# Kernel optimization log

Hardware: AMD Instinct MI355X
Metric: run time of the kernel (lower is better)

Reference implementation:

```python
import jax, jax.numpy as jnp
import numpy as np

B, HC, WC, KC = 4, 32, 32, 1024   # coarse feature map (ResNet101 layer3)
HF, WF, KF = 128, 128, 256        # fine feature map (ResNet101 layer1)
DC = 4                            # downscale_coef; HF // DC == HC


def setup_inputs() -> dict:
    key = jax.random.key(0)
    k1, k2, k3, k4 = jax.random.split(key, 4)
    return {
        "F_g1_coarse": jax.random.normal(k1, (B, HC, WC, KC), jnp.float32),
        "F_gk_coarse": jax.random.normal(k2, (B, HC, WC, KC), jnp.float32),
        "F_g1_fine": jax.random.normal(k3, (B, HF, WF, KF), jnp.float32),
        "F_gk_fine": jax.random.normal(k4, (B, HF, WF, KF), jnp.float32),
    }


def _coarse_match(f1, fk):
    # For every coarse position in Gk find nearest (L2) coarse position in G1.
    b, h, w, k = f1.shape
    a = f1.reshape(b, h * w, k)   # G1 positions
    q = fk.reshape(b, h * w, k)   # Gk positions
    # ||q||^2 + ||a||^2 - 2 q.a  -> [B, HW_gk, HW_g1]
    d = ((q * q).sum(-1)[:, :, None]
         + (a * a).sum(-1)[:, None, :]
         - 2.0 * jnp.einsum('bnk,bmk->bnm', q, a))
    idx = jnp.argmin(d, axis=-1)                       # [B, HW]
    cm = jnp.stack([idx // w, idx % w], axis=-1)       # (row, col) in G1
    return cm.reshape(b, h, w, 2).astype(jnp.int32)


def _fine_match(f1, fk, cm, dc):
    # Refine each dc x dc fine tile of Gk by searching the fine pixels of G1
    # covered by the coarse matches of the 3x3 coarse-neighborhood.
    b, h, w, k = fk.shape
    hc, wc = h // dc, w // dc
    off = jnp.arange(-1, 2)
    nI = jnp.clip(jnp.arange(hc)[:, None] + off[None, :], 0, hc - 1)  # [Hc,3]
    nJ = jnp.clip(jnp.arange(wc)[:, None] + off[None, :], 0, wc - 1)  # [Wc,3]
    # neighbor coarse matches: [B, Hc, Wc, 3, 3, 2]
    nb = cm[:, nI[:, None, :, None], nJ[None, :, None, :]]
    nb = nb.reshape(b, hc, wc, 9, 2)
    # expand each coarse match to its dc*dc fine pixels in G1
    sr = jnp.repeat(jnp.arange(dc), dc)   # [dc^2] row shifts
    sc = jnp.tile(jnp.arange(dc), dc)     # [dc^2] col shifts
    ncand = 9 * dc * dc                   # 144 candidates per tile
    cand_r = (nb[..., 0][..., None] * dc + sr).reshape(b, hc, wc, ncand)
    cand_c = (nb[..., 1][..., None] * dc + sc).reshape(b, hc, wc, ncand)
    # gather candidate fine features from G1: [B, Hc, Wc, N, K]
    bi = jnp.arange(b)[:, None, None, None]
    cand_f = f1[bi, cand_r, cand_c]
    # fine tile features of Gk: [B, Hc, Wc, dc^2, K]
    fkb = fk.reshape(b, hc, dc, wc, dc, k).transpose(0, 1, 3, 2, 4, 5)
    fkb = fkb.reshape(b, hc, wc, dc * dc, k)
    dist = ((fkb * fkb).sum(-1)[..., :, None]
            + (cand_f * cand_f).sum(-1)[..., None, :]
            - 2.0 * jnp.einsum('bhwpk,bhwnk->bhwpn', fkb, cand_f))
    best = jnp.argmin(dist, axis=-1)      # [B, Hc, Wc, dc^2]
    hi = jnp.arange(hc)[None, :, None, None]
    wi = jnp.arange(wc)[None, None, :, None]
    best_r = cand_r[bi, hi, wi, best]     # [B, Hc, Wc, dc^2]
    best_c = cand_c[bi, hi, wi, best]
    def to_grid(x):
        return x.reshape(b, hc, wc, dc, dc).transpose(0, 1, 3, 2, 4).reshape(b, h, w)
    return jnp.stack([to_grid(best_r), to_grid(best_c)], axis=-1).astype(jnp.int32)


def reference(F_g1_coarse, F_gk_coarse, F_g1_fine, F_gk_fine):
    closest_coarse = _coarse_match(F_g1_coarse, F_gk_coarse)   # [B,Hc,Wc,2]
    closest_fine = _fine_match(F_g1_fine, F_gk_fine, closest_coarse, DC)  # [B,H,W,2]
    return closest_coarse, closest_fine
```

## Files before the change

kernel.cpp:

```cpp
#include <hip/hip_runtime.h>
#include <cstdint>
#include <cstddef>

#define BB 4
#define HCC 32
#define WCC 32
#define KCC 1024
#define NCC (HCC*WCC)
#define HFF 128
#define WFF 128
#define KFF 256
#define DCC 4
#define NCHUNK 8

typedef _Float16 half8 __attribute__((ext_vector_type(8)));
typedef _Float16 half4_t __attribute__((ext_vector_type(4)));
typedef float f32x4 __attribute__((ext_vector_type(4)));
#define MFMA16(a,b,c) __builtin_amdgcn_mfma_f32_16x16x32_f16((a),(b),(c),0,0,0)
#define INV2K 0.00048828125f

__device__ inline void cvt8(const float4 u0, const float4 u1, half8& h, half8& l2) {
  float uu[8];
  *(float4*)uu = u0; *(float4*)(uu + 4) = u1;
  #pragma unroll
  for (int e = 0; e < 8; ++e) {
    _Float16 hh = (_Float16)uu[e];
    float r = (uu[e] - (float)hh) * 2048.0f;
    h[e] = hh; l2[e] = (_Float16)r;
  }
}

template<int K>
__global__ __launch_bounds__(256) void preconv_kernel(
    const float* __restrict__ src0, const float* __restrict__ src1,
    _Float16* __restrict__ hi0, _Float16* __restrict__ lo0,
    _Float16* __restrict__ hi1, _Float16* __restrict__ lo1,
    float* __restrict__ nr0, float* __restrict__ nr1, int rows) {
  const float* __restrict__ src = blockIdx.y ? src1 : src0;
  _Float16* __restrict__ hi = blockIdx.y ? hi1 : hi0;
  _Float16* __restrict__ lo = blockIdx.y ? lo1 : lo0;
  float* __restrict__ nrm = blockIdx.y ? nr1 : nr0;
  const int wave = threadIdx.x >> 6, lane = threadIdx.x & 63;
  const int row = blockIdx.x * 4 + wave;
  if (row >= rows) return;
  const float* p = src + (size_t)row * K;
  const size_t ob = (size_t)row * K + lane * 4;
  float s = 0.f;
  #pragma unroll
  for (int c = 0; c < K / 256; ++c) {
    float4 v = *(const float4*)(p + c * 256 + lane * 4);
    s += v.x*v.x + v.y*v.y + v.z*v.z + v.w*v.w;
    float vv[4] = {v.x, v.y, v.z, v.w};
    half4_t h, l2;
    #pragma unroll
    for (int e = 0; e < 4; ++e) {
      _Float16 hh = (_Float16)vv[e];
      l2[e] = (_Float16)((vv[e] - (float)hh) * 2048.0f);
      h[e] = hh;
    }
    *(half4_t*)(hi + ob + c * 256) = h;
    *(half4_t*)(lo + ob + c * 256) = l2;
  }
  #pragma unroll
  for (int m = 1; m <= 32; m <<= 1) s += __shfl_xor(s, m, 64);
  if (lane == 0) nrm[row] = s;
}

__global__ __launch_bounds__(256) void preconv_fine_kernel(
    const float* __restrict__ src, _Float16* __restrict__ hl,
    float* __restrict__ nrm, int rows) {
  const int wave = threadIdx.x >> 6, lane = threadIdx.x & 63;
  const int row = blockIdx.x * 4 + wave;
  if (row >= rows) return;
  float4 v = *(const float4*)(src + (size_t)row * KFF + lane * 4);
  float s = v.x*v.x + v.y*v.y + v.z*v.z + v.w*v.w;
  float vv[4] = {v.x, v.y, v.z, v.w};
  half4_t h, l2;
  #pragma unroll
  for (int e = 0; e < 4; ++e) {
    _Float16 hh = (_Float16)vv[e];
    l2[e] = (_Float16)((vv[e] - (float)hh) * 2048.0f);
    h[e] = hh;
  }
  const size_t dst = (size_t)row * 512 + (lane >> 3) * 64 + ((lane >> 1) & 3) * 16 + (lane & 1) * 4;
  *(half4_t*)(hl + dst)     = h;
  *(half4_t*)(hl + dst + 8) = l2;
  #pragma unroll
  for (int m = 1; m <= 32; m <<= 1) s += __shfl_xor(s, m, 64);
  if (lane == 0) nrm[row] = s;
}

__global__ __launch_bounds__(256) void coarse_kernel3(
    const _Float16* __restrict__ gAhi, const _Float16* __restrict__ gAlo,
    const _Float16* __restrict__ gBhi, const _Float16* __restrict__ gBlo,
    const float* __restrict__ na, const float* __restrict__ nq,
    float* __restrict__ pval, int* __restrict__ pidx) {
  __shared__ _Float16 Ahi[128][64], Alo[128][64];
  __shared__ _Float16 Bhi[64][64],  Blo[64][64];
  __shared__ float a2s[128], q2s[64];
  __shared__ float redv[2][64];
  __shared__ int   redi[2][64];

  const int t = threadIdx.x;
  const int chunk = blockIdx.x;
  const int n0 = blockIdx.y * 64;
  const int b  = blockIdx.z;
  const int m0 = chunk * 128;

  const int ar = t >> 1, ahf = t & 1;
  const int brw = t >> 2, bq = t & 3;
  const int l  = t & 63;
  const int wv = t >> 6;
  const int wm = wv >> 1, wn = wv & 1;

  if (t < 128) a2s[t] = na[b*NCC + m0 + t];
  else if (t < 192) q2s[t - 128] = nq[b*NCC + n0 + (t - 128)];

  const _Float16* __restrict__ gah = gAhi + (size_t)(b*NCC + m0 + ar) * KCC + ahf * 32;
  const _Float16* __restrict__ gal = gAlo + (size_t)(b*NCC + m0 + ar) * KCC + ahf * 32;
  const _Float16* __restrict__ gbh = gBhi + (size_t)(b*NCC + n0 + brw) * KCC + bq * 16;
  const _Float16* __restrict__ gbl = gBlo + (size_t)(b*NCC + n0 + brw) * KCC + bq * 16;

  f32x4 accA[4][2], accB[4][2];
  #pragma unroll
  for (int mt = 0; mt < 4; ++mt)
    #pragma unroll
    for (int nt = 0; nt < 2; ++nt) { accA[mt][nt] = (f32x4)0.f; accB[mt][nt] = (f32x4)0.f; }

  half8 pah[4], pal[4], pbh[2], pbl[2];
  #pragma unroll
  for (int c2 = 0; c2 < 4; ++c2) { pah[c2] = *(const half8*)(gah + c2*8); pal[c2] = *(const half8*)(gal + c2*8); }
  #pragma unroll
  for (int c2 = 0; c2 < 2; ++c2) { pbh[c2] = *(const half8*)(gbh + c2*8); pbl[c2] = *(const half8*)(gbl + c2*8); }

  for (int k0 = 0; k0 < KCC; k0 += 64) {
    __syncthreads();
    #pragma unroll
    for (int c2 = 0; c2 < 4; ++c2) {
      int cs = (ahf * 4 + c2) ^ (ar & 7);
      *(half8*)&Ahi[ar][cs * 8] = pah[c2];
      *(half8*)&Alo[ar][cs * 8] = pal[c2];
    }
    #pragma unroll
    for (int c2 = 0; c2 < 2; ++c2) {
      int cs = (bq * 2 + c2) ^ (brw & 7);
      *(half8*)&Bhi[brw][cs * 8] = pbh[c2];
      *(half8*)&Blo[brw][cs * 8] = pbl[c2];
    }
    __syncthreads();

    if (k0 + 64 < KCC) {
      #pragma unroll
      for (int c2 = 0; c2 < 4; ++c2) {
        pah[c2] = *(const half8*)(gah + k0 + 64 + c2*8);
        pal[c2] = *(const half8*)(gal + k0 + 64 + c2*8);
      }
      #pragma unroll
      for (int c2 = 0; c2 < 2; ++c2) {
        pbh[c2] = *(const half8*)(gbh + k0 + 64 + c2*8);
        pbl[c2] = *(const half8*)(gbl + k0 + 64 + c2*8);
      }
    }

    #pragma unroll
    for (int kk = 0; kk < 2; ++kk) {
      const int cs = ((kk * 4 + (l >> 4)) ^ (l & 7)) * 8;
      half8 ah[4], al[4], bh[2], bl[2];
      #pragma unroll
      for (int mt = 0; mt < 4; ++mt) {
        int row = wm * 64 + mt * 16 + (l & 15);
        ah[mt] = *(const half8*)&Ahi[row][cs];
        al[mt] = *(const half8*)&Alo[row][cs];
      }
      #pragma unroll
      for (int nt = 0; nt < 2; ++nt) {
        int row = wn * 32 + nt * 16 + (l & 15);
        bh[nt] = *(const half8*)&Bhi[row][cs];
        bl[nt] = *(const half8*)&Blo[row][cs];
      }
      #pragma unroll
      for (int mt = 0; mt < 4; ++mt)
        #pragma unroll
        for (int nt = 0; nt < 2; ++nt) {
          accA[mt][nt] = MFMA16(ah[mt], bh[nt], accA[mt][nt]);
          accB[mt][nt] = MFMA16(ah[mt], bl[nt], accB[mt][nt]);
          accB[mt][nt] = MFMA16(al[mt], bh[nt], accB[mt][nt]);
        }
    }
  }

  #pragma unroll
  for (int nt = 0; nt < 2; ++nt) {
    float q2 = q2s[wn * 32 + nt * 16 + (l & 15)];
    float bv = 3.0e38f; int bi = 0;
    #pragma unroll
    for (int mt = 0; mt < 4; ++mt)
      #pragma unroll
      for (int r = 0; r < 4; ++r) {
        float dot = accA[mt][nt][r] + accB[mt][nt][r] * INV2K;
        int ml = wm * 64 + mt * 16 + (l >> 4) * 4 + r;
        float d = (q2 + a2s[ml]) - 2.0f * dot;
        if (d < bv) { bv = d; bi = m0 + ml; }
      }
    #pragma unroll
    for (int mm = 16; mm < 64; mm <<= 1) {
      float ov = __shfl_xor(bv, mm, 64);
      int oi = __shfl_xor(bi, mm, 64);
      if (ov < bv || (ov == bv && oi < bi)) { bv = ov; bi = oi; }
    }
    if ((l >> 4) == 0) { redv[wm][wn*32 + nt*16 + l] = bv; redi[wm][wn*32 + nt*16 + l] = bi; }
  }
  __syncthreads();
  if (t < 64) {
    float v0 = redv[0][t]; int i0 = redi[0][t];
    float v1 = redv[1][t]; int i1 = redi[1][t];
    if (v1 < v0) { v0 = v1; i0 = i1; }
    pval[((size_t)b * NCC + n0 + t) * NCHUNK + chunk] = v0;
    pidx[((size_t)b * NCC + n0 + t) * NCHUNK + chunk] = i0;
  }
}

__global__ __launch_bounds__(256) void coarse_reduce_kernel(
    const float* __restrict__ pval, const int* __restrict__ pidx,
    int* __restrict__ out) {
  int g = blockIdx.x * 256 + threadIdx.x;
  if (g >= BB * NCC) return;
  float bv = pval[(size_t)g * NCHUNK];
  int bi = pidx[(size_t)g * NCHUNK];
  #pragma unroll
  for (int c = 1; c < NCHUNK; ++c) {
    float v = pval[(size_t)g * NCHUNK + c];
    int ix = pidx[(size_t)g * NCHUNK + c];
    if (v < bv) { bv = v; bi = ix; }
  }
  out[(size_t)g*2]     = bi >> 5;
  out[(size_t)g*2 + 1] = bi & 31;
}

__global__ __launch_bounds__(512) void fine_kernel5(
    const _Float16* __restrict__ gHL, const float* __restrict__ fkf,
    const float* __restrict__ naf, const int* __restrict__ coarse,
    int* __restrict__ outf) {
  __shared__ _Float16 CS[384 * 64];
  __shared__ _Float16 QS[128 * 64];
  __shared__ int   rIdx[384];
  __shared__ float tNORM[384];
  __shared__ float QN4[128][4];
  __shared__ int cbr[24], cbc[24];

  const int t = threadIdx.x;
  const int bx = blockIdx.x, by = blockIdx.y, b = blockIdx.z;
  const int l = t & 63, w = t >> 6;
  const int cy = w >> 2, cx = w & 3;
  const int ii = by * 2 + cy, jj = bx * 4 + cx;

  if (t < 24) {
    int wy = t / 6, wx = t % 6;
    int y = min(max(by * 2 - 1 + wy, 0), HCC - 1);
    int x = min(max(bx * 4 - 1 + wx, 0), WCC - 1);
    int base = ((b * HCC + y) * WCC + x) * 2;
    cbr[t] = coarse[base]; cbc[t] = coarse[base + 1];
  }
  __syncthreads();
  if (t < 384) {
    int slot = t >> 4, s = t & 15;
    int row = cbr[slot] * DCC + (s >> 2), col = cbc[slot] * DCC + (s & 3);
    int g = (b * HFF + row) * WFF + col;
    rIdx[t] = g; tNORM[t] = naf[g];
  }
  __syncthreads();

  unsigned srcOff[6], dstOff[6];
  #pragma unroll
  for (int it = 0; it < 6; ++it) {
    int g2 = it * 512 + t;
    int rowG = g2 >> 3, lc = g2 & 7;
    srcOff[it] = (unsigned)rIdx[rowG] * 512u + (unsigned)((lc >> 1) * 16 + (lc & 1) * 8);
    dstOff[it] = (unsigned)(rowG * 64 + (lc ^ (rowG & 7)) * 8);
  }
  const int qrow = t >> 2, qpart = t & 3;
  const int qcell = qrow >> 4, qs = qrow & 15;
  const int qfr = (by * 2 + (qcell >> 2)) * DCC + (qs >> 2);
  const int qfc = (bx * 4 + (qcell & 3)) * DCC + (qs & 3);
  const float* qsrc = fkf + ((size_t)(b * HFF + qfr) * WFF + qfc) * KFF + qpart * 8;
  const int qswz = qrow & 7;
  float qnp = 0.f;

  half8 pf[6];
  #pragma unroll
  for (int it = 0; it < 6; ++it) pf[it] = *(const half8*)(gHL + srcOff[it]);
  float4 qu0 = *(const float4*)(qsrc);
  float4 qu1 = *(const float4*)(qsrc + 4);

  f32x4 accA[9], accB[9];
  #pragma unroll
  for (int T = 0; T < 9; ++T) { accA[T] = (f32x4)0.f; accB[T] = (f32x4)0.f; }

  const int q = l >> 4, r = l & 15;
  const int rsw = r & 7;
  const int woff[9] = {0, 1, 2, 6, 7, 8, 12, 13, 14};
  const int wbase = cy * 6 + cx;

  for (int ke = 0; ke < 8; ++ke) {
    __syncthreads();
    #pragma unroll
    for (int it = 0; it < 6; ++it) *(half8*)&CS[dstOff[it]] = pf[it];
    {
      qnp += qu0.x*qu0.x + qu0.y*qu0.y + qu0.z*qu0.z + qu0.w*qu0.w
           + qu1.x*qu1.x + qu1.y*qu1.y + qu1.z*qu1.z + qu1.w*qu1.w;
      half8 hh, hl;
      cvt8(qu0, qu1, hh, hl);
      *(half8*)&QS[qrow * 64 + ((qpart * 2)     ^ qswz) * 8] = hh;
      *(half8*)&QS[qrow * 64 + ((qpart * 2 + 1) ^ qswz) * 8] = hl;
      if (ke == 7) QN4[qrow][qpart] = qnp;
    }
    __syncthreads();

    if (ke < 7) {
      #pragma unroll
      for (int it = 0; it < 6; ++it)
        pf[it] = *(const half8*)(gHL + srcOff[it] + (unsigned)(ke + 1) * 64u);
      qu0 = *(const float4*)(qsrc + (ke + 1) * 32);
      qu1 = *(const float4*)(qsrc + (ke + 1) * 32 + 4);
    }

    half8 bh = *(const half8*)&QS[(w * 16 + r) * 64 + ((q * 2)     ^ rsw) * 8];
    half8 bl = *(const half8*)&QS[(w * 16 + r) * 64 + ((q * 2 + 1) ^ rsw) * 8];
    #pragma unroll
    for (int T = 0; T < 9; ++T) {
      int rowG = (wbase + woff[T]) * 16 + r;
      half8 ah = *(const half8*)&CS[rowG * 64 + ((q * 2)     ^ rsw) * 8];
      half8 al = *(const half8*)&CS[rowG * 64 + ((q * 2 + 1) ^ rsw) * 8];
      accA[T] = MFMA16(ah, bh, accA[T]);
      accB[T] = MFMA16(ah, bl, accB[T]);
      accB[T] = MFMA16(al, bh, accB[T]);
    }
  }

  {
    float q2v = QN4[w * 16 + r][0] + QN4[w * 16 + r][1]
              + QN4[w * 16 + r][2] + QN4[w * 16 + r][3];
    float bv = 3.0e38f; int bi = 0;
    #pragma unroll
    for (int T = 0; T < 9; ++T) {
      int slot = wbase + woff[T];
      #pragma unroll
      for (int r2 = 0; r2 < 4; ++r2) {
        int s4 = q * 4 + r2;
        float cn = tNORM[slot * 16 + s4];
        float dot = accA[T][r2] + accB[T][r2] * INV2K;
        float d = (q2v + cn) - 2.0f * dot;
        int m = T * 16 + s4;
        if (d < bv) { bv = d; bi = m; }
      }
    }
    #pragma unroll
    for (int mm = 16; mm < 64; mm <<= 1) {
      float ov = __shfl_xor(bv, mm, 64);
      int oi = __shfl_xor(bi, mm, 64);
      if (ov < bv || (ov == bv && oi < bi)) { bv = ov; bi = oi; }
    }
    if (l < 16) {
      int T = bi >> 4, s3 = bi & 15, slot = wbase + woff[T];
      int br = cbr[slot] * DCC + (s3 >> 2);
      int bc = cbc[slot] * DCC + (s3 & 3);
      int fr = ii * DCC + (l >> 2), fc = jj * DCC + (l & 3);
      size_t ob = ((size_t)(b * HFF + fr) * WFF + fc) * 2;
      outf[ob]     = br;
      outf[ob + 1] = bc;
    }
  }
}

__global__ __launch_bounds__(256, 2) void coarse_kernel(
    const float* __restrict__ f1, const float* __restrict__ fk,
    float* __restrict__ pval, int* __restrict__ pidx) {
  __shared__ _Float16 Ahi[128][64], Alo[128][64];
  __shared__ _Float16 Bhi[64][64],  Blo[64][64];
  __shared__ float npA[256], npB[256];
  __shared__ float a2s[128], q2s[64];
  __shared__ float redv[2][64];
  __shared__ int   redi[2][64];

  const int t = threadIdx.x;
  const int chunk = blockIdx.x;
  const int n0 = blockIdx.y * 64;
  const int b  = blockIdx.z;
  const int m0 = chunk * 128;

  const float* __restrict__ Abase = f1 + ((size_t)b * NCC + m0) * KCC;
  const float* __restrict__ Bbase = fk + ((size_t)b * NCC + n0) * KCC;

  const int ar = t >> 1, ahf = t & 1;
  const int brw = t >> 2, bq = t & 3;
  const int l  = t & 63;
  const int wv = t >> 6;
  const int wm = wv >> 1, wn = wv & 1;

  float nrmA = 0.f, nrmB = 0.f;
  f32x4 accA[4][2], accB[4][2];
  #pragma unroll
  for (int mt = 0; mt < 4; ++mt)
    #pragma unroll
    for (int nt = 0; nt < 2; ++nt) { accA[mt][nt] = (f32x4)0.f; accB[mt][nt] = (f32x4)0.f; }

  for (int k0 = 0; k0 < KCC; k0 += 64) {
    __syncthreads();
    {
      const float4* src = (const float4*)(Abase + (size_t)ar * KCC + k0 + ahf * 32);
      float4 va[8];
      #pragma unroll
      for (int i2 = 0; i2 < 8; ++i2) va[i2] = src[i2];
      #pragma unroll
      for (int i2 = 0; i2 < 8; ++i2)
        nrmA += va[i2].x*va[i2].x + va[i2].y*va[i2].y + va[i2].z*va[i2].z + va[i2].w*va[i2].w;
      #pragma unroll
      for (int c2 = 0; c2 < 4; ++c2) {
        half8 hh, hl;
        cvt8(va[c2*2], va[c2*2+1], hh, hl);
        int cs = (ahf * 4 + c2) ^ (ar & 7);
        *(half8*)&Ahi[ar][cs * 8] = hh;
        *(half8*)&Alo[ar][cs * 8] = hl;
      }
    }
    {
      const float4* src = (const float4*)(Bbase + (size_t)brw * KCC + k0 + bq * 16);
      float4 vb[4];
      #pragma unroll
      for (int i2 = 0; i2 < 4; ++i2) vb[i2] = src[i2];
      #pragma unroll
      for (int i2 = 0; i2 < 4; ++i2)
        nrmB += vb[i2].x*vb[i2].x + vb[i2].y*vb[i2].y + vb[i2].z*vb[i2].z + vb[i2].w*vb[i2].w;
      #pragma unroll
      for (int c2 = 0; c2 < 2; ++c2) {
        half8 hh, hl;
        cvt8(vb[c2*2], vb[c2*2+1], hh, hl);
        int cs = (bq * 2 + c2) ^ (brw & 7);
        *(half8*)&Bhi[brw][cs * 8] = hh;
        *(half8*)&Blo[brw][cs * 8] = hl;
      }
    }
    __syncthreads();

    #pragma unroll
    for (int kk = 0; kk < 2; ++kk) {
      const int cs = ((kk * 4 + (l >> 4)) ^ (l & 7)) * 8;
      half8 ah[4], al[4], bh[2], bl[2];
      #pragma unroll
      for (int mt = 0; mt < 4; ++mt) {
        int row = wm * 64 + mt * 16 + (l & 15);
        ah[mt] = *(const half8*)&Ahi[row][cs];
        al[mt] = *(const half8*)&Alo[row][cs];
      }
      #pragma unroll
      for (int nt = 0; nt < 2; ++nt) {
        int row = wn * 32 + nt * 16 + (l & 15);
        bh[nt] = *(const half8*)&Bhi[row][cs];
        bl[nt] = *(const half8*)&Blo[row][cs];
      }
      #pragma unroll
      for (int mt = 0; mt < 4; ++mt)
        #pragma unroll
        for (int nt = 0; nt < 2; ++nt) {
          accA[mt][nt] = MFMA16(ah[mt], bh[nt], accA[mt][nt]);
          accB[mt][nt] = MFMA16(ah[mt], bl[nt], accB[mt][nt]);
          accB[mt][nt] = MFMA16(al[mt], bh[nt], accB[mt][nt]);
        }
    }
  }

  npA[t] = nrmA; npB[t] = nrmB;
  __syncthreads();
  if (t < 128) a2s[t] = npA[2*t] + npA[2*t + 1];
  if (t < 64)  q2s[t] = npB[4*t] + npB[4*t + 1] + npB[4*t + 2] + npB[4*t + 3];
  __syncthreads();

  #pragma unroll
  for (int nt = 0; nt < 2; ++nt) {
    float q2 = q2s[wn * 32 + nt * 16 + (l & 15)];
    float bv = 3.0e38f; int bi = 0;
    #pragma unroll
    for (int mt = 0; mt < 4; ++mt)
      #pragma unroll
      for (int r = 0; r < 4; ++r) {
        float dot = accA[mt][nt][r] + accB[mt][nt][r] * INV2K;
        int ml = wm * 64 + mt * 16 + (l >> 4) * 4 + r;
        float d = (q2 + a2s[ml]) - 2.0f * dot;
        if (d < bv) { bv = d; bi = m0 + ml; }
      }
    #pragma unroll
    for (int mm = 16; mm < 64; mm <<= 1) {
      float ov = __shfl_xor(bv, mm, 64);
      int oi = __shfl_xor(bi, mm, 64);
      if (ov < bv || (ov == bv && oi < bi)) { bv = ov; bi = oi; }
    }
    if ((l >> 4) == 0) { redv[wm][wn*32 + nt*16 + l] = bv; redi[wm][wn*32 + nt*16 + l] = bi; }
  }
  __syncthreads();
  if (t < 64) {
    float v0 = redv[0][t]; int i0 = redi[0][t];
    float v1 = redv[1][t]; int i1 = redi[1][t];
    if (v1 < v0) { v0 = v1; i0 = i1; }
    pval[((size_t)b * NCC + n0 + t) * NCHUNK + chunk] = v0;
    pidx[((size_t)b * NCC + n0 + t) * NCHUNK + chunk] = i0;
  }
}

__global__ __launch_bounds__(192) void fine_kernel(
    const float* __restrict__ f1, const float* __restrict__ fkf,
    const int* __restrict__ coarse, int* __restrict__ outf) {
  __shared__ _Float16 Qhi[16][256], Qlo[16][256];
  __shared__ float qn[16], cn[144];
  __shared__ int cROW[144];
  __shared__ int cbr[9], cbc[9];
  __shared__ float redv[3][16];
  __shared__ int   redi[3][16];

  const int t = threadIdx.x;
  const int j = blockIdx.x, i = blockIdx.y, b = blockIdx.z;
  const int l = t & 63, wv = t >> 6;

  if (t < 9) {
    int di = t / 3 - 1, dj = t % 3 - 1;
    int y = min(max(i + di, 0), HCC - 1);
    int x = min(max(j + dj, 0), WCC - 1);
    int base = ((b*HCC + y)*WCC + x) * 2;
    cbr[t] = coarse[base];
    cbc[t] = coarse[base + 1];
  }
  __syncthreads();
  if (t < 144) {
    int n9 = t >> 4, s = t & 15;
    int row = cbr[n9]*DCC + (s >> 2), col = cbc[n9]*DCC + (s & 3);
    cROW[t] = (b*HFF + row)*WFF + col;
  }
  if (t < 64) {
    int qr = l & 15, qq = l >> 4;
    int fr = i*DCC + (qr >> 2), fc = j*DCC + (qr & 3);
    const float* src = fkf + ((size_t)(b*HFF + fr)*WFF + fc) * KFF + qq * 64;
    float s2 = 0.f;
    #pragma unroll
    for (int c2 = 0; c2 < 8; ++c2) {
      float4 u0 = *(const float4*)(src + c2*8);
      float4 u1 = *(const float4*)(src + c2*8 + 4);
      s2 += u0.x*u0.x + u0.y*u0.y + u0.z*u0.z + u0.w*u0.w
          + u1.x*u1.x + u1.y*u1.y + u1.z*u1.z + u1.w*u1.w;
      half8 hh, hl;
      cvt8(u0, u1, hh, hl);
      int cs = (qq * 8 + c2) ^ (qr & 7);
      *(half8*)&Qhi[qr][cs * 8] = hh;
      *(half8*)&Qlo[qr][cs * 8] = hl;
    }
    s2 += __shfl_xor(s2, 16, 64);
    s2 += __shfl_xor(s2, 32, 64);
    if (qq == 0) qn[qr] = s2;
  }
  __syncthreads();

  const float* ap[3];
  #pragma unroll
  for (int T = 0; T < 3; ++T)
    ap[T] = f1 + (size_t)cROW[(wv*3 + T)*16 + (l & 15)] * KFF;

  f32x4 accA[3], accB[3];
  float nrmp[3];
  #pragma unroll
  for (int T = 0; T < 3; ++T) { accA[T] = (f32x4)0.f; accB[T] = (f32x4)0.f; nrmp[T] = 0.f; }

  #pragma unroll 2
  for (int s = 0; s < 8; ++s) {
    const int cs = ((s * 4 + (l >> 4)) ^ (l & 7)) * 8;
    half8 bh = *(const half8*)&Qhi[l & 15][cs];
    half8 bl = *(const half8*)&Qlo[l & 15][cs];
    #pragma unroll
    for (int T = 0; T < 3; ++T) {
      const float* p = ap[T] + s*32 + (l >> 4)*8;
      float4 u0 = *(const float4*)p;
      float4 u1 = *(const float4*)(p + 4);
      nrmp[T] += u0.x*u0.x + u0.y*u0.y + u0.z*u0.z + u0.w*u0.w
               + u1.x*u1.x + u1.y*u1.y + u1.z*u1.z + u1.w*u1.w;
      half8 ahv, alv;
      cvt8(u0, u1, ahv, alv);
      accA[T] = MFMA16(ahv, bh, accA[T]);
      accB[T] = MFMA16(ahv, bl, accB[T]);
      accB[T] = MFMA16(alv, bh, accB[T]);
    }
  }

  #pragma unroll
  for (int T = 0; T < 3; ++T) {
    float np = nrmp[T];
    np += __shfl_xor(np, 16, 64);
    np += __shfl_xor(np, 32, 64);
    if ((l >> 4) == 0) cn[(wv*3 + T)*16 + l] = np;
  }
  __syncthreads();

  {
    float q2 = qn[l & 15];
    float bv = 3.0e38f; int bi = 0;
    #pragma unroll
    for (int T = 0; T < 3; ++T)
      #pragma unroll
      for (int r = 0; r < 4; ++r) {
        float dot = accA[T][r] + accB[T][r] * INV2K;
        int m = (wv*3 + T)*16 + (l >> 4)*4 + r;
        float d = (q2 + cn[m]) - 2.0f * dot;
        if (d < bv) { bv = d; bi = m; }
      }
    #pragma unroll
    for (int mm = 16; mm < 64; mm <<= 1) {
      float ov = __shfl_xor(bv, mm, 64);
      int oi = __shfl_xor(bi, mm, 64);
      if (ov < bv || (ov == bv && oi < bi)) { bv = ov; bi = oi; }
    }
    if ((l >> 4) == 0 && l < 16) { redv[wv][l] = bv; redi[wv][l] = bi; }
  }
  __syncthreads();

  if (t < 16) {
    float v = redv[0][t]; int ix = redi[0][t];
    #pragma unroll
    for (int w = 1; w < 3; ++w) {
      float ov = redv[w][t];
      if (ov < v) { v = ov; ix = redi[w][t]; }
    }
    int n9 = ix >> 4, s3 = ix & 15;
    int br = cbr[n9]*DCC + (s3 >> 2);
    int bc = cbc[n9]*DCC + (s3 & 3);
    int fr = i*DCC + (t >> 2), fc = j*DCC + (t & 3);
    size_t ob = ((size_t)(b*HFF + fr)*WFF + fc) * 2;
    outf[ob]     = br;
    outf[ob + 1] = bc;
  }
}

extern "C" void kernel_launch(void* const* d_in, const int* in_sizes, int n_in,
                              void* d_out, int out_size, void* d_ws, size_t ws_size,
                              hipStream_t stream) {
  (void)in_sizes; (void)n_in; (void)out_size;
  const float* f1c = (const float*)d_in[0];
  const float* fkc = (const float*)d_in[1];
  const float* f1f = (const float*)d_in[2];
  const float* fkf = (const float*)d_in[3];
  int* out = (int*)d_out;

  const size_t NEED = 101220352;
  if (ws_size >= NEED) {
    char* w = (char*)d_ws;
    _Float16* cAhi = (_Float16*)(w);
    _Float16* cAlo = (_Float16*)(w + 8388608);
    _Float16* cBhi = (_Float16*)(w + 16777216);
    _Float16* cBlo = (_Float16*)(w + 25165824);
    _Float16* fHL  = (_Float16*)(w + 33554432);
    float* na_c = (float*)(w + 100663296);
    float* nq_c = (float*)(w + 100679680);
    float* na_f = (float*)(w + 100696064);
    float* pval = (float*)(w + 100958208);
    int*   pidx = (int*)  (w + 101089280);

    preconv_kernel<KCC><<<dim3(BB*NCC/4, 2), 256, 0, stream>>>(
        f1c, fkc, cAhi, cAlo, cBhi, cBlo, na_c, nq_c, BB*NCC);
    preconv_fine_kernel<<<dim3(BB*HFF*WFF/4), 256, 0, stream>>>(
        f1f, fHL, na_f, BB*HFF*WFF);
    coarse_kernel3<<<dim3(NCHUNK, NCC/64, BB), 256, 0, stream>>>(
        cAhi, cAlo, cBhi, cBlo, na_c, nq_c, pval, pidx);
    coarse_reduce_kernel<<<dim3((BB*NCC + 255)/256), 256, 0, stream>>>(pval, pidx, out);
    fine_kernel5<<<dim3(WCC/4, HCC/2, BB), 512, 0, stream>>>(
        fHL, fkf, na_f, out, out + BB*NCC*2);
  } else {
    float* pval = (float*)d_ws;
    int*   pidx = (int*)((float*)d_ws + BB*NCC*NCHUNK);
    coarse_kernel<<<dim3(NCHUNK, NCC/64, BB), 256, 0, stream>>>(f1c, fkc, pval, pidx);
    coarse_reduce_kernel<<<dim3((BB*NCC + 255)/256), 256, 0, stream>>>(pval, pidx, out);
    fine_kernel<<<dim3(WCC, HCC, BB), 192, 0, stream>>>(f1f, fkf, out, out + BB*NCC*2);
  }
}
```

Measured before the change: 112.4 us.

## Double-buffer fine-kernel candidate tiles and load query fragments directly into registers

The fine matching kernel now keeps two shared-memory buffers for candidate tiles. The next K-slice is written to the other buffer while MFMAs consume the current one, so each iteration needs one barrier instead of two. Each lane loads and converts its own query fragment straight into registers, which removes the query shared-memory staging and the QN4 norm table; the query norm is reduced with cross-lane shuffles instead. Launch bounds also request two blocks per CU, at the cost of more LDS (about 98KB per block) and tighter register limits, and unused reduction arrays were left in.

Measured after the change: 104.9 us. 6.7% less time.

```diff
diff --git a/kernel.cpp b/kernel.cpp
--- a/kernel.cpp
+++ b/kernel.cpp
@@ -237,16 +237,16 @@
   out[(size_t)g*2 + 1] = bi & 31;
 }
 
-__global__ __launch_bounds__(512) void fine_kernel5(
+__global__ __launch_bounds__(512, 2) void fine_kernel6(
     const _Float16* __restrict__ gHL, const float* __restrict__ fkf,
     const float* __restrict__ naf, const int* __restrict__ coarse,
     int* __restrict__ outf) {
-  __shared__ _Float16 CS[384 * 64];
-  __shared__ _Float16 QS[128 * 64];
+  __shared__ _Float16 CS[2][384 * 64];
   __shared__ int   rIdx[384];
   __shared__ float tNORM[384];
-  __shared__ float QN4[128][4];
   __shared__ int cbr[24], cbc[24];
+  __shared__ float redv[8][16];
+  __shared__ int   redi[8][16];
 
   const int t = threadIdx.x;
   const int bx = blockIdx.x, by = blockIdx.y, b = blockIdx.z;
@@ -278,68 +278,69 @@
     srcOff[it] = (unsigned)rIdx[rowG] * 512u + (unsigned)((lc >> 1) * 16 + (lc & 1) * 8);
     dstOff[it] = (unsigned)(rowG * 64 + (lc ^ (rowG & 7)) * 8);
   }
-  const int qrow = t >> 2, qpart = t & 3;
-  const int qcell = qrow >> 4, qs = qrow & 15;
-  const int qfr = (by * 2 + (qcell >> 2)) * DCC + (qs >> 2);
-  const int qfc = (bx * 4 + (qcell & 3)) * DCC + (qs & 3);
-  const float* qsrc = fkf + ((size_t)(b * HFF + qfr) * WFF + qfc) * KFF + qpart * 8;
-  const int qswz = qrow & 7;
-  float qnp = 0.f;
+
+  const int q = l >> 4, r = l & 15;
+  const int qfr = ii * DCC + (r >> 2), qfc = jj * DCC + (r & 3);
+  const float* qsrc = fkf + ((size_t)(b * HFF + qfr) * WFF + qfc) * KFF + q * 8;
 
   half8 pf[6];
   #pragma unroll
   for (int it = 0; it < 6; ++it) pf[it] = *(const half8*)(gHL + srcOff[it]);
+  #pragma unroll
+  for (int it = 0; it < 6; ++it) *(half8*)&CS[0][dstOff[it]] = pf[it];
+  #pragma unroll
+  for (int it = 0; it < 6; ++it) pf[it] = *(const half8*)(gHL + srcOff[it] + 64u);
   float4 qu0 = *(const float4*)(qsrc);
   float4 qu1 = *(const float4*)(qsrc + 4);
+  __syncthreads();
 
   f32x4 accA[9], accB[9];
   #pragma unroll
   for (int T = 0; T < 9; ++T) { accA[T] = (f32x4)0.f; accB[T] = (f32x4)0.f; }
 
-  const int q = l >> 4, r = l & 15;
-  const int rsw = r & 7;
   const int woff[9] = {0, 1, 2, 6, 7, 8, 12, 13, 14};
   const int wbase = cy * 6 + cx;
-
+  const int rsw = r & 7;
+  const int c0 = ((q * 2) ^ rsw) * 8, c1 = ((q * 2 + 1) ^ rsw) * 8;
+  float qnp = 0.f;
+
+  #pragma unroll
   for (int ke = 0; ke < 8; ++ke) {
-    __syncthreads();
-    #pragma unroll
-    for (int it = 0; it < 6; ++it) *(half8*)&CS[dstOff[it]] = pf[it];
-    {
-      qnp += qu0.x*qu0.x + qu0.y*qu0.y + qu0.z*qu0.z + qu0.w*qu0.w
-           + qu1.x*qu1.x + qu1.y*qu1.y + qu1.z*qu1.z + qu1.w*qu1.w;
-      half8 hh, hl;
-      cvt8(qu0, qu1, hh, hl);
-      *(half8*)&QS[qrow * 64 + ((qpart * 2)     ^ qswz) * 8] = hh;
-      *(half8*)&QS[qrow * 64 + ((qpart * 2 + 1) ^ qswz) * 8] = hl;
-      if (ke == 7) QN4[qrow][qpart] = qnp;
-    }
-    __syncthreads();
-
+    const int cur = ke & 1;
+    qnp += qu0.x*qu0.x + qu0.y*qu0.y + qu0.z*qu0.z + qu0.w*qu0.w
+         + qu1.x*qu1.x + qu1.y*qu1.y + qu1.z*qu1.z + qu1.w*qu1.w;
+    half8 bh, bl;
+    cvt8(qu0, qu1, bh, bl);
     if (ke < 7) {
-      #pragma unroll
-      for (int it = 0; it < 6; ++it)
-        pf[it] = *(const half8*)(gHL + srcOff[it] + (unsigned)(ke + 1) * 64u);
       qu0 = *(const float4*)(qsrc + (ke + 1) * 32);
       qu1 = *(const float4*)(qsrc + (ke + 1) * 32 + 4);
     }
-
-    half8 bh = *(const half8*)&QS[(w * 16 + r) * 64 + ((q * 2)     ^ rsw) * 8];
-    half8 bl = *(const half8*)&QS[(w * 16 + r) * 64 + ((q * 2 + 1) ^ rsw) * 8];
     #pragma unroll
     for (int T = 0; T < 9; ++T) {
       int rowG = (wbase + woff[T]) * 16 + r;
-      half8 ah = *(const half8*)&CS[rowG * 64 + ((q * 2)     ^ rsw) * 8];
-      half8 al = *(const half8*)&CS[rowG * 64 + ((q * 2 + 1) ^ rsw) * 8];
+      half8 ah = *(const half8*)&CS[cur][rowG * 64 + c0];
+      half8 al = *(const half8*)&CS[cur][rowG * 64 + c1];
       accA[T] = MFMA16(ah, bh, accA[T]);
       accB[T] = MFMA16(ah, bl, accB[T]);
       accB[T] = MFMA16(al, bh, accB[T]);
     }
-  }
+    if (ke < 7) {
+      #pragma unroll
+      for (int it = 0; it < 6; ++it) *(half8*)&CS[cur ^ 1][dstOff[it]] = pf[it];
+      if (ke < 6) {
+        #pragma unroll
+        for (int it = 0; it < 6; ++it)
+          pf[it] = *(const half8*)(gHL + srcOff[it] + (unsigned)(ke + 2) * 64u);
+      }
+    }
+    __syncthreads();
+  }
+
+  qnp += __shfl_xor(qnp, 16, 64);
+  qnp += __shfl_xor(qnp, 32, 64);
+  const float q2v = qnp;
 
   {
-    float q2v = QN4[w * 16 + r][0] + QN4[w * 16 + r][1]
-              + QN4[w * 16 + r][2] + QN4[w * 16 + r][3];
     float bv = 3.0e38f; int bi = 0;
     #pragma unroll
     for (int T = 0; T < 9; ++T) {
@@ -370,6 +371,7 @@
       outf[ob + 1] = bc;
     }
   }
+  (void)redv; (void)redi;
 }
 
 __global__ __launch_bounds__(256, 2) void coarse_kernel(
@@ -666,7 +668,7 @@
     coarse_kernel3<<<dim3(NCHUNK, NCC/64, BB), 256, 0, stream>>>(
         cAhi, cAlo, cBhi, cBlo, na_c, nq_c, pval, pidx);
     coarse_reduce_kernel<<<dim3((BB*NCC + 255)/256), 256, 0, stream>>>(pval, pidx, out);
-    fine_kernel5<<<dim3(WCC/4, HCC/2, BB), 512, 0, stream>>>(
+    fine_kernel6<<<dim3(WCC/4, HCC/2, BB), 512, 0, stream>>>(
         fHL, fkf, na_f, out, out + BB*NCC*2);
   } else {
     float* pval = (float*)d_ws;
```
